# Kernel optimization log

Hardware: AMD Instinct MI355X
Metric: run time of the kernel (lower is better)

Reference implementation:

```python
import jax, jax.numpy as jnp
import numpy as np

N = 100000          # nodes
E = 1600000         # edges
F_IN = 128          # in_channels
C = 32              # hidden_channels (per head)
H = 4               # heads
NEG_SLOPE = 0.2     # PyG GATConv default leaky_relu slope


def setup_inputs() -> dict:
    key = jax.random.key(0)
    ks = jax.random.split(key, 6)
    x = jax.random.normal(ks[0], (N, F_IN), dtype=jnp.float32)
    edge_index = jax.random.randint(ks[1], (2, E), 0, N, dtype=jnp.int32)
    # learned params (PyG GATConv: lin weight, att_src, att_dst, bias)
    W = jax.random.normal(ks[2], (F_IN, H * C), dtype=jnp.float32) * (1.0 / np.sqrt(F_IN))
    att_src = jax.random.normal(ks[3], (H, C), dtype=jnp.float32) * 0.1
    att_dst = jax.random.normal(ks[4], (H, C), dtype=jnp.float32) * 0.1
    bias = jnp.zeros((H * C,), dtype=jnp.float32)
    return {"x": x, "edge_index": edge_index, "W": W,
            "att_src": att_src, "att_dst": att_dst, "bias": bias}


def reference(x, edge_index, W, att_src, att_dst, bias):
    # linear projection, split into heads: [N, H, C]
    h = (x @ W).reshape(N, H, C)
    # per-node attention terms: [N, H]
    a_src = jnp.einsum('nhc,hc->nh', h, att_src)
    a_dst = jnp.einsum('nhc,hc->nh', h, att_dst)
    src, dst = edge_index[0], edge_index[1]
    # edge-wise logits: [E, H]
    alpha = jax.nn.leaky_relu(a_src[src] + a_dst[dst], NEG_SLOPE)
    # segment softmax over incoming edges of each dst node
    amax = jax.ops.segment_max(alpha, dst, num_segments=N)       # [N, H]
    amax = jnp.where(jnp.isfinite(amax), amax, 0.0)
    ex = jnp.exp(alpha - amax[dst])                              # [E, H]
    denom = jax.ops.segment_sum(ex, dst, num_segments=N)         # [N, H]
    alpha = ex / (denom[dst] + 1e-16)                            # [E, H]
    # weighted messages, scatter-add to dst: [N, H, C]
    msg = h[src] * alpha[:, :, None]
    out = jax.ops.segment_sum(msg, dst, num_segments=N)
    out = out.reshape(N, H * C) + bias
    return jax.nn.elu(out)
```

## Files before the change

kernel.cpp:

```cpp
#include <hip/hip_runtime.h>
#include <hip/hip_bf16.h>
#include <math.h>

#define N_NODES 100000
#define N_EDGES 1600000
#define NEG_SLOPE 0.2f

#define NB_BUCKET 782
#define ST_CAP 2560

#define OFF_H     0
#define OFF_ASRC  25600000
#define OFF_ADST  27200000
#define OFF_NODE  28800000
#define OFF_BCUR  29600000
#define OFF_TMP   29604096
#define OFF_WHT   37611776
#define OFF_WLT   37644544
#define OFF_WAH   37677312
#define OFF_WAL   37681408

typedef __attribute__((ext_vector_type(8))) __bf16 bf16x8;
typedef __attribute__((ext_vector_type(4))) float  f32x4;
union BF8 { unsigned u32[4]; bf16x8 v; };

__device__ __forceinline__ float leaky(float x) {
    return fmaxf(x, NEG_SLOPE * x);
}
__device__ __forceinline__ float sel4(int h, float a, float b, float c, float d) {
    return h == 0 ? a : (h == 1 ? b : (h == 2 ? c : d));
}
__device__ __forceinline__ float2 bf2_to_f2(unsigned int u) {
    float2 r;
    r.x = __uint_as_float(u << 16);
    r.y = __uint_as_float(u & 0xffff0000u);
    return r;
}
__device__ __forceinline__ unsigned bf16_rne(float f) {
    const unsigned b = __float_as_uint(f);
    return ((b + 0x7FFFu + ((b >> 16) & 1u)) >> 16) & 0xFFFFu;
}
__device__ __forceinline__ float bf16_tof(unsigned hb) {
    return __uint_as_float(hb << 16);
}
__device__ __forceinline__ void wave_lds_fence() {
    asm volatile("s_waitcnt lgkmcnt(0)" ::: "memory");
    __builtin_amdgcn_sched_barrier(0);
}

__global__ __launch_bounds__(256) void wprep_kernel(
    const float* __restrict__ W, const float* __restrict__ att_src,
    const float* __restrict__ att_dst,
    ushort* __restrict__ WhT, ushort* __restrict__ WlT,
    ushort* __restrict__ WAh, ushort* __restrict__ WAl,
    int* __restrict__ bcur)
{
    const int idx = blockIdx.x * 256 + threadIdx.x;
    const int n = idx >> 7, k = idx & 127;
    const float w  = W[k * 128 + n];
    const unsigned hb = bf16_rne(w);
    const float rs = w - bf16_tof(hb);
    WhT[n * 128 + k] = (ushort)hb;
    WlT[n * 128 + k] = (ushort)bf16_rne(rs);

    if (idx < 2048) {
        const int j = idx >> 7;
        float v = 0.f;
        if (j < 8) {
            const int hh = j & 3;
            const float* att = (j < 4) ? att_src : att_dst;
#pragma unroll
            for (int c = 0; c < 32; ++c)
                v = fmaf(W[k * 128 + hh * 32 + c], att[hh * 32 + c], v);
        }
        const unsigned ab = bf16_rne(v);
        WAh[j * 128 + k] = (ushort)ab;
        WAl[j * 128 + k] = (ushort)bf16_rne(v - bf16_tof(ab));
    }
    if (idx < NB_BUCKET) bcur[idx] = 0;
}

#define S1_EPB 6250
#define FAT_SCAT_BLOCKS 256
#define FAT_GEMM_BLOCKS 782

__global__ __launch_bounds__(256, 2) void fat_kernel(
    const float* __restrict__ x, const ushort* __restrict__ WhT,
    const ushort* __restrict__ WlT, const ushort* __restrict__ WAh,
    const ushort* __restrict__ WAl,
    ushort* __restrict__ h_u16, float* __restrict__ a_src, float* __restrict__ a_dst,
    const int* __restrict__ src, const int* __restrict__ dst,
    int* __restrict__ bcur, unsigned int* __restrict__ tmp)
{
    __shared__ int s_cnt[NB_BUCKET];
    __shared__ int s_dstash[S1_EPB];

    const int tid = threadIdx.x;

    if (blockIdx.x < FAT_SCAT_BLOCKS) {
        for (int i = tid; i < NB_BUCKET; i += 256) s_cnt[i] = 0;
        __syncthreads();
        const int e0 = blockIdx.x * S1_EPB;
        for (int i = tid; i < S1_EPB; i += 256) {
            const int d = dst[e0 + i];
            s_dstash[i] = d;
            atomicAdd(&s_cnt[d >> 7], 1);
        }
        __syncthreads();
        for (int b = tid; b < NB_BUCKET; b += 256) {
            const int c = s_cnt[b];
            s_cnt[b] = c ? (b * ST_CAP + atomicAdd(&bcur[b], c)) : 0;
        }
        __syncthreads();
        for (int i = tid; i < S1_EPB; i += 256) {
            const int d = s_dstash[i];
            const int s = src[e0 + i];
            const int p = atomicAdd(&s_cnt[d >> 7], 1);
            tmp[p] = ((unsigned int)s << 7) | (unsigned int)(d & 127);
        }
        return;
    }

    const int gb   = blockIdx.x - FAT_SCAT_BLOCKS;
    const int wv   = tid >> 6;
    const int lane = tid & 63;
    const int c15  = lane & 15;
    const int kg   = lane >> 4;
    const int r0g  = gb * 128 + wv * 32;

    bf16x8 ah[2][4], al[2][4];
#pragma unroll
    for (int mt = 0; mt < 2; ++mt) {
        int row = r0g + mt * 16 + c15;
        row = row < N_NODES ? row : N_NODES - 1;
        const float4* xp = (const float4*)&x[(size_t)row * 128];
#pragma unroll
        for (int ks = 0; ks < 4; ++ks) {
            const int kb = ks * 32 + kg * 8;
            const float4 fa = xp[kb >> 2];
            const float4 fb = xp[(kb >> 2) + 1];
            const float f[8] = {fa.x, fa.y, fa.z, fa.w, fb.x, fb.y, fb.z, fb.w};
            BF8 H, L;
#pragma unroll
            for (int j = 0; j < 4; ++j) {
                const unsigned h0 = bf16_rne(f[2 * j + 0]);
                const unsigned h1 = bf16_rne(f[2 * j + 1]);
                const unsigned l0 = bf16_rne(f[2 * j + 0] - bf16_tof(h0));
                const unsigned l1 = bf16_rne(f[2 * j + 1] - bf16_tof(h1));
                H.u32[j] = h0 | (h1 << 16);
                L.u32[j] = l0 | (l1 << 16);
            }
            ah[mt][ks] = H.v;
            al[mt][ks] = L.v;
        }
    }

    f32x4 acc[2][8];
    f32x4 acca[2];
#pragma unroll
    for (int mt = 0; mt < 2; ++mt) {
        acca[mt] = (f32x4){0.f, 0.f, 0.f, 0.f};
#pragma unroll
        for (int nt = 0; nt < 8; ++nt)
            acc[mt][nt] = (f32x4){0.f, 0.f, 0.f, 0.f};
    }

#pragma unroll
    for (int ks = 0; ks < 4; ++ks) {
        const int kb = ks * 32 + kg * 8;
#pragma unroll
        for (int nt = 0; nt < 8; ++nt) {
            const int col = nt * 16 + c15;
            const bf16x8 bh = *(const bf16x8*)&WhT[col * 128 + kb];
            const bf16x8 bl = *(const bf16x8*)&WlT[col * 128 + kb];
            acc[0][nt] = __builtin_amdgcn_mfma_f32_16x16x32_bf16(ah[0][ks], bh, acc[0][nt], 0, 0, 0);
            acc[1][nt] = __builtin_amdgcn_mfma_f32_16x16x32_bf16(ah[1][ks], bh, acc[1][nt], 0, 0, 0);
            acc[0][nt] = __builtin_amdgcn_mfma_f32_16x16x32_bf16(al[0][ks], bh, acc[0][nt], 0, 0, 0);
            acc[1][nt] = __builtin_amdgcn_mfma_f32_16x16x32_bf16(al[1][ks], bh, acc[1][nt], 0, 0, 0);
            acc[0][nt] = __builtin_amdgcn_mfma_f32_16x16x32_bf16(ah[0][ks], bl, acc[0][nt], 0, 0, 0);
            acc[1][nt] = __builtin_amdgcn_mfma_f32_16x16x32_bf16(ah[1][ks], bl, acc[1][nt], 0, 0, 0);
        }
        const bf16x8 bha = *(const bf16x8*)&WAh[c15 * 128 + kb];
        const bf16x8 bla = *(const bf16x8*)&WAl[c15 * 128 + kb];
        acca[0] = __builtin_amdgcn_mfma_f32_16x16x32_bf16(ah[0][ks], bha, acca[0], 0, 0, 0);
        acca[1] = __builtin_amdgcn_mfma_f32_16x16x32_bf16(ah[1][ks], bha, acca[1], 0, 0, 0);
        acca[0] = __builtin_amdgcn_mfma_f32_16x16x32_bf16(al[0][ks], bha, acca[0], 0, 0, 0);
        acca[1] = __builtin_amdgcn_mfma_f32_16x16x32_bf16(al[1][ks], bha, acca[1], 0, 0, 0);
        acca[0] = __builtin_amdgcn_mfma_f32_16x16x32_bf16(ah[0][ks], bla, acca[0], 0, 0, 0);
        acca[1] = __builtin_amdgcn_mfma_f32_16x16x32_bf16(ah[1][ks], bla, acca[1], 0, 0, 0);
    }

#pragma unroll
    for (int mt = 0; mt < 2; ++mt) {
#pragma unroll
        for (int reg = 0; reg < 4; ++reg) {
            const int row = r0g + mt * 16 + kg * 4 + reg;
            if (row >= N_NODES) continue;
#pragma unroll
            for (int nt = 0; nt < 8; ++nt)
                h_u16[(size_t)row * 128 + nt * 16 + c15] =
                    (ushort)bf16_rne(acc[mt][nt][reg]);
            if (c15 < 4)
                a_src[row * 4 + c15] = acca[mt][reg];
            else if (c15 < 8)
                a_dst[row * 4 + (c15 - 4)] = acca[mt][reg];
        }
    }
}

__global__ __launch_bounds__(256) void phaseB_kernel(
    const unsigned int* __restrict__ tmp, const int* __restrict__ bcur,
    int2* __restrict__ node_info, int* __restrict__ csr)
{
    __shared__ unsigned int st[ST_CAP];
    __shared__ int hist[128];
    __shared__ int cur[128];
    __shared__ int wtot[4];

    const int b    = blockIdx.x;
    const int tid  = threadIdx.x;
    const int lane = tid & 63;
    const int wv   = tid >> 6;
    const int base = b * ST_CAP;
    int cnt = bcur[b];
    cnt = cnt < ST_CAP ? cnt : ST_CAP;

    if (tid < 128) hist[tid] = 0;
    __syncthreads();

    for (int i = tid; i < cnt; i += 256) {
        const unsigned int v = tmp[base + i];
        st[i] = v;
        atomicAdd(&hist[v & 127], 1);
    }
    __syncthreads();

    const int hv = (tid < 128) ? hist[tid] : 0;
    int sv = hv;
#pragma unroll
    for (int off = 1; off < 64; off <<= 1) {
        int u = __shfl_up(sv, off);
        if (lane >= off) sv += u;
    }
    if (lane == 63) wtot[wv] = sv;
    __syncthreads();
    const int wpre = (wv > 0 ? wtot[0] : 0) + (wv > 1 ? wtot[1] : 0) + (wv > 2 ? wtot[2] : 0);
    if (tid < 128) {
        const int excl = wpre + sv - hv;
        cur[tid] = excl;
        const int node = (b << 7) + tid;
        if (node < N_NODES) node_info[node] = make_int2(base + excl, hv);
    }
    __syncthreads();

    for (int i = tid; i < cnt; i += 256) {
        const unsigned int v = st[i];
        const int p = atomicAdd(&cur[v & 127], 1);
        csr[base + p] = (int)(v >> 7);
    }
}

__global__ __launch_bounds__(256, 4) void gat_agg_kernel(
    const int* __restrict__ csr_src, const int2* __restrict__ node_info,
    const __hip_bfloat162* __restrict__ h_bf,
    const float* __restrict__ a_src, const float* __restrict__ a_dst,
    const float* __restrict__ bias, float* __restrict__ out)
{
    __shared__ float4 stage[4][128];

    const int wv   = threadIdx.x >> 6;
    const int lane = threadIdx.x & 63;
    const int node = blockIdx.x * 4 + wv;

    const int2 nf  = node_info[node];
    const int start = nf.x;
    const int deg   = nf.y;

    const float4 ad4 = ((const float4*)a_dst)[node];

    float sf = __int_as_float(0);
    float e0 = 0.f, e1 = 0.f, e2 = 0.f, e3 = 0.f;
    if (lane < deg) {
        const int s = csr_src[start + lane];
        sf = __int_as_float(s);
        const float4 as4 = ((const float4*)a_src)[s];
        e0 = __expf(leaky(as4.x + ad4.x));
        e1 = __expf(leaky(as4.y + ad4.y));
        e2 = __expf(leaky(as4.z + ad4.z));
        e3 = __expf(leaky(as4.w + ad4.w));
    }
    stage[wv][lane * 2 + 0] = make_float4(sf, e0, sf, e1);
    stage[wv][lane * 2 + 1] = make_float4(sf, e2, sf, e3);
    wave_lds_fence();

    if (deg <= 64) {
        const int qw   = lane >> 4;
        const int cpos = lane & 15;
        const int hsub = cpos >> 2;
        const float2* sp = (const float2*)&stage[wv][0];
        const uint4*  hp = (const uint4*)h_bf;

        float acc[8];
#pragma unroll
        for (int i = 0; i < 8; ++i) acc[i] = 0.f;
        float den = 0.f;

        for (int j = 0; j < deg; j += 16) {
#pragma unroll
            for (int u = 0; u < 4; ++u) {
                const float2 se = sp[(j + u * 4 + qw) * 4 + hsub];
                const float ev = se.y;
                const unsigned s = (unsigned)__float_as_int(se.x);
                const uint4 hv = hp[(size_t)(s * 16u + (unsigned)cpos)];
                float2 f;
                f = bf2_to_f2(hv.x);
                acc[0] = fmaf(ev, f.x, acc[0]);
                acc[1] = fmaf(ev, f.y, acc[1]);
                f = bf2_to_f2(hv.y);
                acc[2] = fmaf(ev, f.x, acc[2]);
                acc[3] = fmaf(ev, f.y, acc[3]);
                f = bf2_to_f2(hv.z);
                acc[4] = fmaf(ev, f.x, acc[4]);
                acc[5] = fmaf(ev, f.y, acc[5]);
                f = bf2_to_f2(hv.w);
                acc[6] = fmaf(ev, f.x, acc[6]);
                acc[7] = fmaf(ev, f.y, acc[7]);
                den += ev;
            }
        }

#pragma unroll
        for (int i = 0; i < 8; ++i) acc[i] += __shfl_xor(acc[i], 16);
#pragma unroll
        for (int i = 0; i < 8; ++i) acc[i] += __shfl_xor(acc[i], 32);
        den += __shfl_xor(den, 16);
        den += __shfl_xor(den, 32);

        const float inv = 1.0f / (den + 1e-16f);
#pragma unroll
        for (int i = 0; i < 8; ++i) acc[i] *= inv;

        if (qw == 0) {
            float4* sf4 = (float4*)&stage[wv][0];
            sf4[cpos * 2 + 0] = make_float4(acc[0], acc[1], acc[2], acc[3]);
            sf4[cpos * 2 + 1] = make_float4(acc[4], acc[5], acc[6], acc[7]);
        }
        wave_lds_fence();
        const float2 v  = ((const float2*)&stage[wv][0])[lane];
        const float2 b2 = ((const float2*)bias)[lane];
        float ox = v.x + b2.x;
        float oy = v.y + b2.y;
        ox = ox > 0.f ? ox : __expf(ox) - 1.f;
        oy = oy > 0.f ? oy : __expf(oy) - 1.f;
        ((float2*)out)[(size_t)node * 64 + lane] = make_float2(ox, oy);
    } else {
        const int hidx = lane >> 4;
        const float adh = sel4(hidx, ad4.x, ad4.y, ad4.z, ad4.w);
        float2 acc = {0.f, 0.f};
        float  den = 0.f;
        for (int j = 0; j < deg; ++j) {
            const int s = csr_src[start + j];
            const float ash = a_src[s * 4 + hidx];
            const float ex = __expf(leaky(ash + adh));
            const float2 f = __bfloat1622float2(h_bf[(size_t)s * 64 + lane]);
            acc.x += ex * f.x;
            acc.y += ex * f.y;
            den   += ex;
        }
        const float inv = 1.0f / (den + 1e-16f);
        const float2 b2 = ((const float2*)bias)[lane];
        float ox = acc.x * inv + b2.x;
        float oy = acc.y * inv + b2.y;
        ox = ox > 0.f ? ox : expm1f(ox);
        oy = oy > 0.f ? oy : expm1f(oy);
        ((float2*)out)[(size_t)node * 64 + lane] = make_float2(ox, oy);
    }
}

extern "C" void kernel_launch(void* const* d_in, const int* in_sizes, int n_in,
                              void* d_out, int out_size, void* d_ws, size_t ws_size,
                              hipStream_t stream)
{
    const float* x       = (const float*)d_in[0];
    const int*   ei      = (const int*)  d_in[1];
    const float* W       = (const float*)d_in[2];
    const float* att_src = (const float*)d_in[3];
    const float* att_dst = (const float*)d_in[4];
    const float* bias    = (const float*)d_in[5];
    float*       out     = (float*)d_out;

    char* ws = (char*)d_ws;
    ushort* h_u16 = (ushort*)(ws + OFF_H);
    __hip_bfloat162* h_bf = (__hip_bfloat162*)(ws + OFF_H);
    float* a_src = (float*)(ws + OFF_ASRC);
    float* a_dst = (float*)(ws + OFF_ADST);
    int2*  ninfo = (int2*) (ws + OFF_NODE);
    int*   bcur  = (int*)  (ws + OFF_BCUR);
    unsigned int* tmp = (unsigned int*)(ws + OFF_TMP);
    int*   csr   = (int*)  (ws + OFF_TMP);
    ushort* WhT  = (ushort*)(ws + OFF_WHT);
    ushort* WlT  = (ushort*)(ws + OFF_WLT);
    ushort* WAh  = (ushort*)(ws + OFF_WAH);
    ushort* WAl  = (ushort*)(ws + OFF_WAL);

    const int* srcp = ei;
    const int* dstp = ei + N_EDGES;

    wprep_kernel<<<64, 256, 0, stream>>>(W, att_src, att_dst, WhT, WlT, WAh, WAl, bcur);

    fat_kernel<<<FAT_SCAT_BLOCKS + FAT_GEMM_BLOCKS, 256, 0, stream>>>(
        x, WhT, WlT, WAh, WAl, h_u16, a_src, a_dst,
        srcp, dstp, bcur, tmp);

    phaseB_kernel<<<NB_BUCKET, 256, 0, stream>>>(tmp, bcur, ninfo, csr);

    gat_agg_kernel<<<N_NODES / 4, 256, 0, stream>>>(
        csr, ninfo, h_bf, a_src, a_dst, bias, out);
}
```

Before: 253.8 us.

## Shrink fat_kernel blocks, interleave scatter and GEMM blocks, raise occupancy

The fused kernel now runs twice as many, half-sized blocks. Each scatter block handles 3125 edges and each GEMM block 64 rows with one 16-row tile per wave. Scatter blocks are interleaved every fourth block ID among the GEMM blocks, so both kinds of work are in flight together instead of all scatter blocks being scheduled first. The x loads and bf16 splitting move inside the k-loop, the LDS dst stash is dropped in favour of re-reading dst from global memory, and launch bounds rise to 4 blocks per CU. Together these are meant to cut register and LDS pressure, lift occupancy and overlap memory-bound scatter with MFMA work, at the cost of a second dst read and less reuse of each weight load.

Result: slower. 273.3 us (+7.7%).

```diff
diff --git a/kernel.cpp b/kernel.cpp
--- a/kernel.cpp
+++ b/kernel.cpp
@@ -80,11 +80,12 @@
     if (idx < NB_BUCKET) bcur[idx] = 0;
 }
 
-#define S1_EPB 6250
-#define FAT_SCAT_BLOCKS 256
-#define FAT_GEMM_BLOCKS 782
-
-__global__ __launch_bounds__(256, 2) void fat_kernel(
+#define S1_EPB 3125
+#define N_SCAT 512
+#define N_GEMM 1563
+#define FAT_BLOCKS 2075
+
+__global__ __launch_bounds__(256, 4) void fat_kernel(
     const float* __restrict__ x, const ushort* __restrict__ WhT,
     const ushort* __restrict__ WlT, const ushort* __restrict__ WAh,
     const ushort* __restrict__ WAl,
@@ -93,19 +94,16 @@
     int* __restrict__ bcur, unsigned int* __restrict__ tmp)
 {
     __shared__ int s_cnt[NB_BUCKET];
-    __shared__ int s_dstash[S1_EPB];
-
+
+    const int bid = blockIdx.x;
     const int tid = threadIdx.x;
 
-    if (blockIdx.x < FAT_SCAT_BLOCKS) {
+    if ((bid & 3) == 3 && (bid >> 2) < N_SCAT) {
         for (int i = tid; i < NB_BUCKET; i += 256) s_cnt[i] = 0;
         __syncthreads();
-        const int e0 = blockIdx.x * S1_EPB;
-        for (int i = tid; i < S1_EPB; i += 256) {
-            const int d = dst[e0 + i];
-            s_dstash[i] = d;
-            atomicAdd(&s_cnt[d >> 7], 1);
-        }
+        const int e0 = (bid >> 2) * S1_EPB;
+        for (int i = tid; i < S1_EPB; i += 256)
+            atomicAdd(&s_cnt[dst[e0 + i] >> 7], 1);
         __syncthreads();
         for (int b = tid; b < NB_BUCKET; b += 256) {
             const int c = s_cnt[b];
@@ -113,7 +111,7 @@
         }
         __syncthreads();
         for (int i = tid; i < S1_EPB; i += 256) {
-            const int d = s_dstash[i];
+            const int d = dst[e0 + i];
             const int s = src[e0 + i];
             const int p = atomicAdd(&s_cnt[d >> 7], 1);
             tmp[p] = ((unsigned int)s << 7) | (unsigned int)(d & 127);
@@ -121,90 +119,70 @@
         return;
     }
 
-    const int gb   = blockIdx.x - FAT_SCAT_BLOCKS;
+    const int gid  = (bid < 2048) ? bid - ((bid + 1) >> 2) : bid - N_SCAT;
     const int wv   = tid >> 6;
     const int lane = tid & 63;
     const int c15  = lane & 15;
     const int kg   = lane >> 4;
-    const int r0g  = gb * 128 + wv * 32;
-
-    bf16x8 ah[2][4], al[2][4];
-#pragma unroll
-    for (int mt = 0; mt < 2; ++mt) {
-        int row = r0g + mt * 16 + c15;
-        row = row < N_NODES ? row : N_NODES - 1;
-        const float4* xp = (const float4*)&x[(size_t)row * 128];
-#pragma unroll
-        for (int ks = 0; ks < 4; ++ks) {
-            const int kb = ks * 32 + kg * 8;
-            const float4 fa = xp[kb >> 2];
-            const float4 fb = xp[(kb >> 2) + 1];
-            const float f[8] = {fa.x, fa.y, fa.z, fa.w, fb.x, fb.y, fb.z, fb.w};
-            BF8 H, L;
-#pragma unroll
-            for (int j = 0; j < 4; ++j) {
-                const unsigned h0 = bf16_rne(f[2 * j + 0]);
-                const unsigned h1 = bf16_rne(f[2 * j + 1]);
-                const unsigned l0 = bf16_rne(f[2 * j + 0] - bf16_tof(h0));
-                const unsigned l1 = bf16_rne(f[2 * j + 1] - bf16_tof(h1));
-                H.u32[j] = h0 | (h1 << 16);
-                L.u32[j] = l0 | (l1 << 16);
-            }
-            ah[mt][ks] = H.v;
-            al[mt][ks] = L.v;
-        }
-    }
-
-    f32x4 acc[2][8];
-    f32x4 acca[2];
-#pragma unroll
-    for (int mt = 0; mt < 2; ++mt) {
-        acca[mt] = (f32x4){0.f, 0.f, 0.f, 0.f};
-#pragma unroll
-        for (int nt = 0; nt < 8; ++nt)
-            acc[mt][nt] = (f32x4){0.f, 0.f, 0.f, 0.f};
-    }
+    const int r0   = gid * 64 + wv * 16;
+
+    int rowl = r0 + c15;
+    rowl = rowl < N_NODES ? rowl : N_NODES - 1;
+    const float4* xp = (const float4*)&x[(size_t)rowl * 128];
+
+    f32x4 acc[8];
+    f32x4 acca = (f32x4){0.f, 0.f, 0.f, 0.f};
+#pragma unroll
+    for (int nt = 0; nt < 8; ++nt)
+        acc[nt] = (f32x4){0.f, 0.f, 0.f, 0.f};
 
 #pragma unroll
     for (int ks = 0; ks < 4; ++ks) {
         const int kb = ks * 32 + kg * 8;
+        const float4 fa = xp[kb >> 2];
+        const float4 fb = xp[(kb >> 2) + 1];
+        const float f[8] = {fa.x, fa.y, fa.z, fa.w, fb.x, fb.y, fb.z, fb.w};
+        BF8 H, L;
+#pragma unroll
+        for (int j = 0; j < 4; ++j) {
+            const unsigned h0 = bf16_rne(f[2 * j + 0]);
+            const unsigned h1 = bf16_rne(f[2 * j + 1]);
+            const unsigned l0 = bf16_rne(f[2 * j + 0] - bf16_tof(h0));
+            const unsigned l1 = bf16_rne(f[2 * j + 1] - bf16_tof(h1));
+            H.u32[j] = h0 | (h1 << 16);
+            L.u32[j] = l0 | (l1 << 16);
+        }
+        const bf16x8 ah = H.v;
+        const bf16x8 al = L.v;
+
 #pragma unroll
         for (int nt = 0; nt < 8; ++nt) {
             const int col = nt * 16 + c15;
             const bf16x8 bh = *(const bf16x8*)&WhT[col * 128 + kb];
             const bf16x8 bl = *(const bf16x8*)&WlT[col * 128 + kb];
-            acc[0][nt] = __builtin_amdgcn_mfma_f32_16x16x32_bf16(ah[0][ks], bh, acc[0][nt], 0, 0, 0);
-            acc[1][nt] = __builtin_amdgcn_mfma_f32_16x16x32_bf16(ah[1][ks], bh, acc[1][nt], 0, 0, 0);
-            acc[0][nt] = __builtin_amdgcn_mfma_f32_16x16x32_bf16(al[0][ks], bh, acc[0][nt], 0, 0, 0);
-            acc[1][nt] = __builtin_amdgcn_mfma_f32_16x16x32_bf16(al[1][ks], bh, acc[1][nt], 0, 0, 0);
-            acc[0][nt] = __builtin_amdgcn_mfma_f32_16x16x32_bf16(ah[0][ks], bl, acc[0][nt], 0, 0, 0);
-            acc[1][nt] = __builtin_amdgcn_mfma_f32_16x16x32_bf16(ah[1][ks], bl, acc[1][nt], 0, 0, 0);
+            acc[nt] = __builtin_amdgcn_mfma_f32_16x16x32_bf16(ah, bh, acc[nt], 0, 0, 0);
+            acc[nt] = __builtin_amdgcn_mfma_f32_16x16x32_bf16(al, bh, acc[nt], 0, 0, 0);
+            acc[nt] = __builtin_amdgcn_mfma_f32_16x16x32_bf16(ah, bl, acc[nt], 0, 0, 0);
         }
         const bf16x8 bha = *(const bf16x8*)&WAh[c15 * 128 + kb];
         const bf16x8 bla = *(const bf16x8*)&WAl[c15 * 128 + kb];
-        acca[0] = __builtin_amdgcn_mfma_f32_16x16x32_bf16(ah[0][ks], bha, acca[0], 0, 0, 0);
-        acca[1] = __builtin_amdgcn_mfma_f32_16x16x32_bf16(ah[1][ks], bha, acca[1], 0, 0, 0);
-        acca[0] = __builtin_amdgcn_mfma_f32_16x16x32_bf16(al[0][ks], bha, acca[0], 0, 0, 0);
-        acca[1] = __builtin_amdgcn_mfma_f32_16x16x32_bf16(al[1][ks], bha, acca[1], 0, 0, 0);
-        acca[0] = __builtin_amdgcn_mfma_f32_16x16x32_bf16(ah[0][ks], bla, acca[0], 0, 0, 0);
-        acca[1] = __builtin_amdgcn_mfma_f32_16x16x32_bf16(ah[1][ks], bla, acca[1], 0, 0, 0);
-    }
-
-#pragma unroll
-    for (int mt = 0; mt < 2; ++mt) {
-#pragma unroll
-        for (int reg = 0; reg < 4; ++reg) {
-            const int row = r0g + mt * 16 + kg * 4 + reg;
-            if (row >= N_NODES) continue;
-#pragma unroll
-            for (int nt = 0; nt < 8; ++nt)
-                h_u16[(size_t)row * 128 + nt * 16 + c15] =
-                    (ushort)bf16_rne(acc[mt][nt][reg]);
-            if (c15 < 4)
-                a_src[row * 4 + c15] = acca[mt][reg];
-            else if (c15 < 8)
-                a_dst[row * 4 + (c15 - 4)] = acca[mt][reg];
-        }
+        acca = __builtin_amdgcn_mfma_f32_16x16x32_bf16(ah, bha, acca, 0, 0, 0);
+        acca = __builtin_amdgcn_mfma_f32_16x16x32_bf16(al, bha, acca, 0, 0, 0);
+        acca = __builtin_amdgcn_mfma_f32_16x16x32_bf16(ah, bla, acca, 0, 0, 0);
+    }
+
+#pragma unroll
+    for (int reg = 0; reg < 4; ++reg) {
+        const int row = r0 + kg * 4 + reg;
+        if (row >= N_NODES) continue;
+#pragma unroll
+        for (int nt = 0; nt < 8; ++nt)
+            h_u16[(size_t)row * 128 + nt * 16 + c15] =
+                (ushort)bf16_rne(acc[nt][reg]);
+        if (c15 < 4)
+            a_src[row * 4 + c15] = acca[reg];
+        else if (c15 < 8)
+            a_dst[row * 4 + (c15 - 4)] = acca[reg];
     }
 }
 
@@ -408,7 +386,7 @@
 
     wprep_kernel<<<64, 256, 0, stream>>>(W, att_src, att_dst, WhT, WlT, WAh, WAl, bcur);
 
-    fat_kernel<<<FAT_SCAT_BLOCKS + FAT_GEMM_BLOCKS, 256, 0, stream>>>(
+    fat_kernel<<<FAT_BLOCKS, 256, 0, stream>>>(
         x, WhT, WlT, WAh, WAl, h_u16, a_src, a_dst,
         srcp, dstp, bcur, tmp);
 
```

## Fuse CSR bucket sort with attention aggregation in one kernel

Applied to the files above, without the earlier changes.

Merges the bucket-sort kernel (phaseB) with the aggregation kernel, so each 512-thread block builds its 128-node CSR slice in shared memory and then aggregates those nodes directly. This removes the global CSR and node_info writes and reads and one kernel launch. In exchange, each wave handles 16 nodes one after another, and the grid drops to 782 large blocks with more LDS each. That cuts parallelism and the latency hiding available for the random h gathers.

Result: slower. 268.0 us (+5.6%).

```diff
diff --git a/kernel.cpp b/kernel.cpp
--- a/kernel.cpp
+++ b/kernel.cpp
@@ -12,7 +12,6 @@
 #define OFF_H     0
 #define OFF_ASRC  25600000
 #define OFF_ADST  27200000
-#define OFF_NODE  28800000
 #define OFF_BCUR  29600000
 #define OFF_TMP   29604096
 #define OFF_WHT   37611776
@@ -208,14 +207,19 @@
     }
 }
 
-__global__ __launch_bounds__(256) void phaseB_kernel(
+__global__ __launch_bounds__(512) void phaseB_agg_kernel(
     const unsigned int* __restrict__ tmp, const int* __restrict__ bcur,
-    int2* __restrict__ node_info, int* __restrict__ csr)
+    const __hip_bfloat162* __restrict__ h_bf,
+    const float* __restrict__ a_src, const float* __restrict__ a_dst,
+    const float* __restrict__ bias, float* __restrict__ out)
 {
     __shared__ unsigned int st[ST_CAP];
+    __shared__ int csr_l[ST_CAP];
     __shared__ int hist[128];
     __shared__ int cur[128];
-    __shared__ int wtot[4];
+    __shared__ int nstart[128];
+    __shared__ int wtot[8];
+    __shared__ float4 stage[8][128];
 
     const int b    = blockIdx.x;
     const int tid  = threadIdx.x;
@@ -228,7 +232,7 @@
     if (tid < 128) hist[tid] = 0;
     __syncthreads();
 
-    for (int i = tid; i < cnt; i += 256) {
+    for (int i = tid; i < cnt; i += 512) {
         const unsigned int v = tmp[base + i];
         st[i] = v;
         atomicAdd(&hist[v & 127], 1);
@@ -242,138 +246,128 @@
         int u = __shfl_up(sv, off);
         if (lane >= off) sv += u;
     }
-    if (lane == 63) wtot[wv] = sv;
+    if (tid < 128 && lane == 63) wtot[wv] = sv;
     __syncthreads();
-    const int wpre = (wv > 0 ? wtot[0] : 0) + (wv > 1 ? wtot[1] : 0) + (wv > 2 ? wtot[2] : 0);
     if (tid < 128) {
+        const int wpre = (wv > 0) ? wtot[0] : 0;
         const int excl = wpre + sv - hv;
-        cur[tid] = excl;
-        const int node = (b << 7) + tid;
-        if (node < N_NODES) node_info[node] = make_int2(base + excl, hv);
+        cur[tid]    = excl;
+        nstart[tid] = excl;
     }
     __syncthreads();
 
-    for (int i = tid; i < cnt; i += 256) {
+    for (int i = tid; i < cnt; i += 512) {
         const unsigned int v = st[i];
         const int p = atomicAdd(&cur[v & 127], 1);
-        csr[base + p] = (int)(v >> 7);
-    }
-}
-
-__global__ __launch_bounds__(256, 4) void gat_agg_kernel(
-    const int* __restrict__ csr_src, const int2* __restrict__ node_info,
-    const __hip_bfloat162* __restrict__ h_bf,
-    const float* __restrict__ a_src, const float* __restrict__ a_dst,
-    const float* __restrict__ bias, float* __restrict__ out)
-{
-    __shared__ float4 stage[4][128];
-
-    const int wv   = threadIdx.x >> 6;
-    const int lane = threadIdx.x & 63;
-    const int node = blockIdx.x * 4 + wv;
-
-    const int2 nf  = node_info[node];
-    const int start = nf.x;
-    const int deg   = nf.y;
-
-    const float4 ad4 = ((const float4*)a_dst)[node];
-
-    float sf = __int_as_float(0);
-    float e0 = 0.f, e1 = 0.f, e2 = 0.f, e3 = 0.f;
-    if (lane < deg) {
-        const int s = csr_src[start + lane];
-        sf = __int_as_float(s);
-        const float4 as4 = ((const float4*)a_src)[s];
-        e0 = __expf(leaky(as4.x + ad4.x));
-        e1 = __expf(leaky(as4.y + ad4.y));
-        e2 = __expf(leaky(as4.z + ad4.z));
-        e3 = __expf(leaky(as4.w + ad4.w));
-    }
-    stage[wv][lane * 2 + 0] = make_float4(sf, e0, sf, e1);
-    stage[wv][lane * 2 + 1] = make_float4(sf, e2, sf, e3);
-    wave_lds_fence();
-
-    if (deg <= 64) {
-        const int qw   = lane >> 4;
-        const int cpos = lane & 15;
-        const int hsub = cpos >> 2;
-        const float2* sp = (const float2*)&stage[wv][0];
-        const uint4*  hp = (const uint4*)h_bf;
-
-        float acc[8];
-#pragma unroll
-        for (int i = 0; i < 8; ++i) acc[i] = 0.f;
-        float den = 0.f;
-
-        for (int j = 0; j < deg; j += 16) {
-#pragma unroll
-            for (int u = 0; u < 4; ++u) {
-                const float2 se = sp[(j + u * 4 + qw) * 4 + hsub];
-                const float ev = se.y;
-                const unsigned s = (unsigned)__float_as_int(se.x);
-                const uint4 hv = hp[(size_t)(s * 16u + (unsigned)cpos)];
-                float2 f;
-                f = bf2_to_f2(hv.x);
-                acc[0] = fmaf(ev, f.x, acc[0]);
-                acc[1] = fmaf(ev, f.y, acc[1]);
-                f = bf2_to_f2(hv.y);
-                acc[2] = fmaf(ev, f.x, acc[2]);
-                acc[3] = fmaf(ev, f.y, acc[3]);
-                f = bf2_to_f2(hv.z);
-                acc[4] = fmaf(ev, f.x, acc[4]);
-                acc[5] = fmaf(ev, f.y, acc[5]);
-                f = bf2_to_f2(hv.w);
-                acc[6] = fmaf(ev, f.x, acc[6]);
-                acc[7] = fmaf(ev, f.y, acc[7]);
-                den += ev;
+        csr_l[p] = (int)(v >> 7);
+    }
+    __syncthreads();
+
+    const float2 b2 = ((const float2*)bias)[lane];
+    const int qw   = lane >> 4;
+    const int cpos = lane & 15;
+    const int hsub = cpos >> 2;
+    const uint4* hp = (const uint4*)h_bf;
+
+    for (int ln = wv * 16; ln < wv * 16 + 16; ++ln) {
+        const int node = (b << 7) + ln;
+        if (node >= N_NODES) break;
+        const int start = nstart[ln];
+        const int deg   = hist[ln];
+
+        const float4 ad4 = ((const float4*)a_dst)[node];
+
+        float sf = __int_as_float(0);
+        float e0 = 0.f, e1 = 0.f, e2 = 0.f, e3 = 0.f;
+        if (lane < deg) {
+            const int s = csr_l[start + lane];
+            sf = __int_as_float(s);
+            const float4 as4 = ((const float4*)a_src)[s];
+            e0 = __expf(leaky(as4.x + ad4.x));
+            e1 = __expf(leaky(as4.y + ad4.y));
+            e2 = __expf(leaky(as4.z + ad4.z));
+            e3 = __expf(leaky(as4.w + ad4.w));
+        }
+        stage[wv][lane * 2 + 0] = make_float4(sf, e0, sf, e1);
+        stage[wv][lane * 2 + 1] = make_float4(sf, e2, sf, e3);
+        wave_lds_fence();
+
+        if (deg <= 64) {
+            const float2* sp = (const float2*)&stage[wv][0];
+
+            float acc[8];
+#pragma unroll
+            for (int i = 0; i < 8; ++i) acc[i] = 0.f;
+            float den = 0.f;
+
+            for (int j = 0; j < deg; j += 16) {
+#pragma unroll
+                for (int u = 0; u < 4; ++u) {
+                    const float2 se = sp[(j + u * 4 + qw) * 4 + hsub];
+                    const float ev = se.y;
+                    const unsigned s = (unsigned)__float_as_int(se.x);
+                    const uint4 hvv = hp[(size_t)(s * 16u + (unsigned)cpos)];
+                    float2 f;
+                    f = bf2_to_f2(hvv.x);
+                    acc[0] = fmaf(ev, f.x, acc[0]);
+                    acc[1] = fmaf(ev, f.y, acc[1]);
+                    f = bf2_to_f2(hvv.y);
+                    acc[2] = fmaf(ev, f.x, acc[2]);
+                    acc[3] = fmaf(ev, f.y, acc[3]);
+                    f = bf2_to_f2(hvv.z);
+                    acc[4] = fmaf(ev, f.x, acc[4]);
+                    acc[5] = fmaf(ev, f.y, acc[5]);
+                    f = bf2_to_f2(hvv.w);
+                    acc[6] = fmaf(ev, f.x, acc[6]);
+                    acc[7] = fmaf(ev, f.y, acc[7]);
+                    den += ev;
+                }
             }
-        }
-
-#pragma unroll
-        for (int i = 0; i < 8; ++i) acc[i] += __shfl_xor(acc[i], 16);
-#pragma unroll
-        for (int i = 0; i < 8; ++i) acc[i] += __shfl_xor(acc[i], 32);
-        den += __shfl_xor(den, 16);
-        den += __shfl_xor(den, 32);
-
-        const float inv = 1.0f / (den + 1e-16f);
-#pragma unroll
-        for (int i = 0; i < 8; ++i) acc[i] *= inv;
-
-        if (qw == 0) {
-            float4* sf4 = (float4*)&stage[wv][0];
-            sf4[cpos * 2 + 0] = make_float4(acc[0], acc[1], acc[2], acc[3]);
-            sf4[cpos * 2 + 1] = make_float4(acc[4], acc[5], acc[6], acc[7]);
-        }
-        wave_lds_fence();
-        const float2 v  = ((const float2*)&stage[wv][0])[lane];
-        const float2 b2 = ((const float2*)bias)[lane];
-        float ox = v.x + b2.x;
-        float oy = v.y + b2.y;
-        ox = ox > 0.f ? ox : __expf(ox) - 1.f;
-        oy = oy > 0.f ? oy : __expf(oy) - 1.f;
-        ((float2*)out)[(size_t)node * 64 + lane] = make_float2(ox, oy);
-    } else {
-        const int hidx = lane >> 4;
-        const float adh = sel4(hidx, ad4.x, ad4.y, ad4.z, ad4.w);
-        float2 acc = {0.f, 0.f};
-        float  den = 0.f;
-        for (int j = 0; j < deg; ++j) {
-            const int s = csr_src[start + j];
-            const float ash = a_src[s * 4 + hidx];
-            const float ex = __expf(leaky(ash + adh));
-            const float2 f = __bfloat1622float2(h_bf[(size_t)s * 64 + lane]);
-            acc.x += ex * f.x;
-            acc.y += ex * f.y;
-            den   += ex;
-        }
-        const float inv = 1.0f / (den + 1e-16f);
-        const float2 b2 = ((const float2*)bias)[lane];
-        float ox = acc.x * inv + b2.x;
-        float oy = acc.y * inv + b2.y;
-        ox = ox > 0.f ? ox : expm1f(ox);
-        oy = oy > 0.f ? oy : expm1f(oy);
-        ((float2*)out)[(size_t)node * 64 + lane] = make_float2(ox, oy);
+
+#pragma unroll
+            for (int i = 0; i < 8; ++i) acc[i] += __shfl_xor(acc[i], 16);
+#pragma unroll
+            for (int i = 0; i < 8; ++i) acc[i] += __shfl_xor(acc[i], 32);
+            den += __shfl_xor(den, 16);
+            den += __shfl_xor(den, 32);
+
+            const float inv = 1.0f / (den + 1e-16f);
+#pragma unroll
+            for (int i = 0; i < 8; ++i) acc[i] *= inv;
+
+            if (qw == 0) {
+                float4* sf4 = (float4*)&stage[wv][0];
+                sf4[cpos * 2 + 0] = make_float4(acc[0], acc[1], acc[2], acc[3]);
+                sf4[cpos * 2 + 1] = make_float4(acc[4], acc[5], acc[6], acc[7]);
+            }
+            wave_lds_fence();
+            const float2 v = ((const float2*)&stage[wv][0])[lane];
+            float ox = v.x + b2.x;
+            float oy = v.y + b2.y;
+            ox = ox > 0.f ? ox : __expf(ox) - 1.f;
+            oy = oy > 0.f ? oy : __expf(oy) - 1.f;
+            ((float2*)out)[(size_t)node * 64 + lane] = make_float2(ox, oy);
+        } else {
+            const int hidx = lane >> 4;
+            const float adh = sel4(hidx, ad4.x, ad4.y, ad4.z, ad4.w);
+            float2 acc = {0.f, 0.f};
+            float  den = 0.f;
+            for (int j = 0; j < deg; ++j) {
+                const int s = csr_l[start + j];
+                const float ash = a_src[s * 4 + hidx];
+                const float ex = __expf(leaky(ash + adh));
+                const float2 f = __bfloat1622float2(h_bf[(size_t)s * 64 + lane]);
+                acc.x += ex * f.x;
+                acc.y += ex * f.y;
+                den   += ex;
+            }
+            const float inv = 1.0f / (den + 1e-16f);
+            float ox = acc.x * inv + b2.x;
+            float oy = acc.y * inv + b2.y;
+            ox = ox > 0.f ? ox : expm1f(ox);
+            oy = oy > 0.f ? oy : expm1f(oy);
+            ((float2*)out)[(size_t)node * 64 + lane] = make_float2(ox, oy);
+        }
     }
 }
 
@@ -394,10 +388,8 @@
     __hip_bfloat162* h_bf = (__hip_bfloat162*)(ws + OFF_H);
     float* a_src = (float*)(ws + OFF_ASRC);
     float* a_dst = (float*)(ws + OFF_ADST);
-    int2*  ninfo = (int2*) (ws + OFF_NODE);
     int*   bcur  = (int*)  (ws + OFF_BCUR);
     unsigned int* tmp = (unsigned int*)(ws + OFF_TMP);
-    int*   csr   = (int*)  (ws + OFF_TMP);
     ushort* WhT  = (ushort*)(ws + OFF_WHT);
     ushort* WlT  = (ushort*)(ws + OFF_WLT);
     ushort* WAh  = (ushort*)(ws + OFF_WAH);
@@ -412,8 +404,6 @@
         x, WhT, WlT, WAh, WAl, h_u16, a_src, a_dst,
         srcp, dstp, bcur, tmp);
 
-    phaseB_kernel<<<NB_BUCKET, 256, 0, stream>>>(tmp, bcur, ninfo, csr);
-
-    gat_agg_kernel<<<N_NODES / 4, 256, 0, stream>>>(
-        csr, ninfo, h_bf, a_src, a_dst, bias, out);
-}
+    phaseB_agg_kernel<<<NB_BUCKET, 512, 0, stream>>>(
+        tmp, bcur, h_bf, a_src, a_dst, bias, out);
+}
```
